# Kernel tuning notes

Measured on AMD Instinct MI355X. Metric: run time of the kernel, lower is better.

## Reference

```python
import jax, jax.numpy as jnp
import numpy as np

N = 4096       # number of graph nodes
F_IN = 512     # in_features == out_features (residual connection requires it)
H = 8          # n_heads


def setup_inputs() -> dict:
    key = jax.random.key(0)
    k1, k2, k3, k4, k5 = jax.random.split(key, 5)
    s = 1.0 / np.sqrt(F_IN)  # keep projections well-scaled
    x = jax.random.normal(k1, (N, F_IN), dtype=jnp.float32)
    Wq = jax.random.normal(k2, (F_IN, F_IN), dtype=jnp.float32) * s
    Wk = jax.random.normal(k3, (F_IN, F_IN), dtype=jnp.float32) * s
    Wv = jax.random.normal(k4, (F_IN, F_IN), dtype=jnp.float32) * s
    adj = jax.random.randint(k5, (H, N, N), 0, 2, dtype=jnp.int32)
    return {"x": x, "Wq": Wq, "Wk": Wk, "Wv": Wv, "adj": adj}


def reference(x, Wq, Wk, Wv, adj):
    # Faithful to torch GraphAttentionLayer.forward (eval mode, dropout off).
    # NOTE: the torch code builds keys = input.repeat(N,1,1).detach() -> the
    # K/V inputs are stop-gradient copies of x; projections are per-node, so
    # we compute them once instead of materializing the redundant [N,N,F].
    n, f = x.shape
    d = f // H  # head dim (chunk_size)
    xk = jax.lax.stop_gradient(x)
    # nn.Linear: y = x @ W.T ; split feature dim into heads -> [H, N, d]
    Q = (x @ Wq.T).reshape(n, H, d).transpose(1, 0, 2)
    K = (xk @ Wk.T).reshape(n, H, d).transpose(1, 0, 2)
    V = (xk @ Wv.T).reshape(n, H, d).transpose(1, 0, 2)
    # scaled by sqrt(in_features) (NOT head dim), as in the original
    scores = jnp.einsum('hnd,hmd->hnm', Q, K) / jnp.sqrt(jnp.float32(f))
    scores = jnp.where(adj > 0, scores, jnp.float32(-9e15))
    attn = jax.nn.softmax(scores, axis=-1)          # [H, N, N]
    out = jnp.einsum('hnm,hmd->hnd', attn, V)       # [H, N, d]
    out = out.transpose(1, 0, 2).reshape(n, f)      # concat heads -> [N, F]
    return jax.nn.elu(out + x)[:, None, :]          # [N, 1, F] like torch
```

## Files before the change

### kernel.cpp

```cpp
#include <hip/hip_runtime.h>
#include <hip/hip_bf16.h>

#define NN 4096
#define FF 512
#define NH 8
#define DH 64

typedef __attribute__((ext_vector_type(8))) short bf16x8;
typedef __attribute__((ext_vector_type(4))) float f32x4;

#define X_OFF  0
#define W_OFF  2097152
#define QF_OFF 2883584
#define KF_OFF 4980736
#define VF_OFF 7077888
#define PACC_OFF 9175040
#define PDEN_USHORT_OFF 17563648
#define PK_USHORT_OFF 17825792

__device__ __forceinline__ ushort f2bf(float f) {
    __hip_bfloat16 h = __float2bfloat16(f);
    return __builtin_bit_cast(ushort, h);
}
__device__ __forceinline__ float bf2f(ushort u) {
    unsigned int v = ((unsigned int)u) << 16;
    return __builtin_bit_cast(float, v);
}

__global__ __launch_bounds__(256) void cvt_kernel(const float* __restrict__ x,
                                                  const float* __restrict__ wq,
                                                  const float* __restrict__ wk,
                                                  const float* __restrict__ wv,
                                                  ushort* __restrict__ ws) {
    int i = blockIdx.x * 256 + threadIdx.x;
    int base = i * 4;
    const float* src;
    int off;
    float sc = 1.f;
    if (base < 2097152) { src = x; off = base; }
    else {
        int t = base - 2097152;
        int m = t >> 18;
        src = (m == 0) ? wq : ((m == 1) ? wk : wv);
        if (m == 0) sc = 0.044194173824159216f;
        off = t & 262143;
    }
    float4 v = *reinterpret_cast<const float4*>(src + off);
    ushort4 o;
    o.x = f2bf(v.x * sc); o.y = f2bf(v.y * sc); o.z = f2bf(v.z * sc); o.w = f2bf(v.w * sc);
    *reinterpret_cast<ushort4*>(ws + base) = o;
}

__global__ __launch_bounds__(256) void packqkv_kernel(const int* __restrict__ adj,
                                                      unsigned int* __restrict__ pk,
                                                      ushort* __restrict__ ws) {
    int bid = blockIdx.x;
    int wave = threadIdx.x >> 6, lane = threadIdx.x & 63;

    if (bid < 8192) {
        int row = bid * 4 + wave;
        const int* ar = adj + (size_t)row * 4096;
        unsigned long long* outp = reinterpret_cast<unsigned long long*>(pk + (size_t)row * 128);
        for (int it = 0; it < 64; it += 4) {
            int v0 = __builtin_nontemporal_load(ar + (it + 0) * 64 + lane);
            int v1 = __builtin_nontemporal_load(ar + (it + 1) * 64 + lane);
            int v2 = __builtin_nontemporal_load(ar + (it + 2) * 64 + lane);
            int v3 = __builtin_nontemporal_load(ar + (it + 3) * 64 + lane);
            unsigned long long b0 = __ballot(v0 != 0);
            unsigned long long b1 = __ballot(v1 != 0);
            unsigned long long b2 = __ballot(v2 != 0);
            unsigned long long b3 = __ballot(v3 != 0);
            if (lane == 0) {
                outp[it + 0] = b0;
                outp[it + 1] = b1;
                outp[it + 2] = b2;
                outp[it + 3] = b3;
            }
        }
        return;
    }

    int q = bid - 8192;
    int mat = q >> 9;
    int rem = q & 511;
    int fb = rem & 7;
    int mb = rem >> 3;
    int la = lane & 15, lk = lane >> 4;

    int m_base = mb * 64 + wave * 16;
    int f_base = fb * 64;

    const ushort* xb = ws + X_OFF;
    const ushort* wb = ws + W_OFF + mat * 262144;

    f32x4 acc[4];
#pragma unroll
    for (int t = 0; t < 4; ++t) acc[t] = (f32x4){0.f, 0.f, 0.f, 0.f};

#pragma unroll 4
    for (int k0 = 0; k0 < 512; k0 += 32) {
        bf16x8 a = *reinterpret_cast<const bf16x8*>(xb + (size_t)(m_base + la) * 512 + k0 + lk * 8);
#pragma unroll
        for (int ft = 0; ft < 4; ++ft) {
            bf16x8 b = *reinterpret_cast<const bf16x8*>(wb + (size_t)(f_base + ft * 16 + la) * 512 + k0 + lk * 8);
            acc[ft] = __builtin_amdgcn_mfma_f32_16x16x32_bf16(a, b, acc[ft], 0, 0, 0);
        }
    }

#pragma unroll
    for (int ft = 0; ft < 4; ++ft) {
#pragma unroll
        for (int r = 0; r < 4; ++r) {
            int n = m_base + lk * 4 + r;
            int d = ft * 16 + la;
            ushort v = f2bf(acc[ft][r]);
            if (mat < 2) {
                ushort* base = ws + (mat == 0 ? QF_OFF : KF_OFF) + (size_t)fb * 262144;
                int blk = n >> 4, rr = n & 15;
                int half = d >> 5, lkk = (d >> 3) & 3, e = d & 7;
                base[(((size_t)blk * 2 + half) * 64 + lkk * 16 + rr) * 8 + e] = v;
            } else {
                ushort* base = ws + VF_OFF + (size_t)fb * 262144;
                int kb64 = n >> 6, kc = n & 63;
                int hf = kc >> 5, lkv = (kc >> 3) & 3, ev = kc & 7;
                int dt = d >> 4, lav = d & 15;
                base[((((size_t)kb64 * 4 + dt) * 2 + hf) * 64 + lkv * 16 + lav) * 8 + ev] = v;
            }
        }
    }
}

__global__ __launch_bounds__(256, 4) void attn_kernel(const unsigned int* __restrict__ pk,
                                                      const ushort* __restrict__ ws,
                                                      ushort* __restrict__ pacc,
                                                      float* __restrict__ pden) {
    __shared__ ushort P[4][16][72];

    int bid = blockIdx.x;
    int h = bid & 7, qb = (bid >> 3) & 63, ks = bid >> 9;
    int wave = threadIdx.x >> 6, lane = threadIdx.x & 63;
    int la = lane & 15, lk = lane >> 4;
    int q0w = qb * 64 + wave * 16;

    const ushort* Qh = ws + QF_OFF + (size_t)h * 262144;
    const ushort* Kh = ws + KF_OFF + (size_t)h * 262144;
    const ushort* Vh = ws + VF_OFF + (size_t)h * 262144;
    const unsigned int* pkh = pk + (size_t)h * 4096 * 128;

    bf16x8 qa0 = *reinterpret_cast<const bf16x8*>(Qh + ((((size_t)(q0w >> 4)) * 2 + 0) * 64 + lane) * 8);
    bf16x8 qa1 = *reinterpret_cast<const bf16x8*>(Qh + ((((size_t)(q0w >> 4)) * 2 + 1) * 64 + lane) * 8);

    f32x4 acc[4];
    float den[4];
    int rowm[4];
#pragma unroll
    for (int r = 0; r < 4; ++r) {
        acc[r] = (f32x4){0.f, 0.f, 0.f, 0.f};
        den[r] = 0.f;
        rowm[r] = (q0w + lk * 4 + r) * 128;
    }

    const f32x4 zero = {0.f, 0.f, 0.f, 0.f};
    int kb0 = ks * 16;

    for (int it = 0; it < 16; ++it) {
        int kb = kb0 + it;

        uint2 mk[4];
#pragma unroll
        for (int r = 0; r < 4; ++r)
            mk[r] = *reinterpret_cast<const uint2*>(pkh + rowm[r] + kb * 2);

        f32x4 s[4];
#pragma unroll
        for (int kt = 0; kt < 4; ++kt) {
            const ushort* kp = Kh + (((size_t)(kb * 4 + kt) * 2) * 64 + lane) * 8;
            bf16x8 kf0 = *reinterpret_cast<const bf16x8*>(kp);
            bf16x8 kf1 = *reinterpret_cast<const bf16x8*>(kp + 512);
            s[kt] = __builtin_amdgcn_mfma_f32_16x16x32_bf16(qa0, kf0, zero, 0, 0, 0);
            s[kt] = __builtin_amdgcn_mfma_f32_16x16x32_bf16(qa1, kf1, s[kt], 0, 0, 0);
        }

#pragma unroll
        for (int kt = 0; kt < 4; ++kt) {
            int sh = la + ((kt & 1) << 4);
#pragma unroll
            for (int r = 0; r < 4; ++r) {
                unsigned int dw = (kt < 2) ? mk[r].x : mk[r].y;
                float sv = ((dw >> sh) & 1u) ? s[kt][r] : -1e30f;
                float e = __expf(sv);
                den[r] += e;
                P[wave][lk * 4 + r][kt * 16 + la] = f2bf(e);
            }
        }

        bf16x8 pa0 = *reinterpret_cast<const bf16x8*>(&P[wave][la][lk * 8]);
        bf16x8 pa1 = *reinterpret_cast<const bf16x8*>(&P[wave][la][32 + lk * 8]);
#pragma unroll
        for (int dt = 0; dt < 4; ++dt) {
            const ushort* vp = Vh + ((((size_t)kb * 4 + dt) * 2) * 64 + lane) * 8;
            bf16x8 vb0 = *reinterpret_cast<const bf16x8*>(vp);
            bf16x8 vb1 = *reinterpret_cast<const bf16x8*>(vp + 512);
            acc[dt] = __builtin_amdgcn_mfma_f32_16x16x32_bf16(pa0, vb0, acc[dt], 0, 0, 0);
            acc[dt] = __builtin_amdgcn_mfma_f32_16x16x32_bf16(pa1, vb1, acc[dt], 0, 0, 0);
        }
    }

#pragma unroll
    for (int r = 0; r < 4; ++r)
#pragma unroll
        for (int mm = 1; mm < 16; mm <<= 1)
            den[r] += __shfl_xor(den[r], mm, 64);

    ushort* pa_out = pacc + ((size_t)ks * 8 + h) * 4096 * 64;
#pragma unroll
    for (int dt = 0; dt < 4; ++dt)
#pragma unroll
        for (int r = 0; r < 4; ++r) {
            int qi = q0w + lk * 4 + r;
            __builtin_nontemporal_store(f2bf(acc[dt][r]), pa_out + (size_t)qi * 64 + dt * 16 + la);
        }
    if (la == 0) {
        float* pd = pden + ((size_t)ks * 8 + h) * 4096;
#pragma unroll
        for (int r = 0; r < 4; ++r)
            pd[q0w + lk * 4 + r] = den[r];
    }
}

__global__ __launch_bounds__(256) void combine_kernel(const float* __restrict__ x,
                                                      const ushort* __restrict__ pacc,
                                                      const float* __restrict__ pden,
                                                      float* __restrict__ out) {
    int idx = blockIdx.x * 256 + threadIdx.x;
    int n = idx >> 7, fq = idx & 127;
    int h = fq >> 4;
    int d4 = (fq & 15) * 4;

    float4 o = make_float4(0.f, 0.f, 0.f, 0.f);
    float den = 0.f;
#pragma unroll
    for (int ksp = 0; ksp < 4; ++ksp) {
        const ushort* pa = pacc + (((size_t)ksp * 8 + h) * 4096 + n) * 64 + d4;
        ushort4 p = *reinterpret_cast<const ushort4*>(pa);
        o.x += bf2f(p.x); o.y += bf2f(p.y); o.z += bf2f(p.z); o.w += bf2f(p.w);
        den += pden[((size_t)ksp * 8 + h) * 4096 + n];
    }
    float4 xv = *reinterpret_cast<const float4*>(x + (size_t)n * 512 + fq * 4);
    float inv = 1.f / den;
    float4 r;
    r.x = o.x * inv + xv.x;
    r.y = o.y * inv + xv.y;
    r.z = o.z * inv + xv.z;
    r.w = o.w * inv + xv.w;
    r.x = (r.x > 0.f) ? r.x : (__expf(r.x) - 1.f);
    r.y = (r.y > 0.f) ? r.y : (__expf(r.y) - 1.f);
    r.z = (r.z > 0.f) ? r.z : (__expf(r.z) - 1.f);
    r.w = (r.w > 0.f) ? r.w : (__expf(r.w) - 1.f);
    *reinterpret_cast<float4*>(out + (size_t)n * 512 + fq * 4) = r;
}

extern "C" void kernel_launch(void* const* d_in, const int* in_sizes, int n_in,
                              void* d_out, int out_size, void* d_ws, size_t ws_size,
                              hipStream_t stream) {
    const float* x  = (const float*)d_in[0];
    const float* wq = (const float*)d_in[1];
    const float* wk = (const float*)d_in[2];
    const float* wv = (const float*)d_in[3];
    const int*   adj = (const int*)d_in[4];
    float* out = (float*)d_out;
    ushort* ws = (ushort*)d_ws;
    ushort* pacc = ws + PACC_OFF;
    float* pden = (float*)(ws + PDEN_USHORT_OFF);
    unsigned int* pk = (unsigned int*)(ws + PK_USHORT_OFF);

    cvt_kernel<<<2816, 256, 0, stream>>>(x, wq, wk, wv, ws);
    packqkv_kernel<<<9728, 256, 0, stream>>>(adj, pk, ws);
    attn_kernel<<<2048, 256, 0, stream>>>(pk, ws, pacc, pden);
    combine_kernel<<<2048, 256, 0, stream>>>(x, pacc, pden, out);
}
```

Measured before the change: 250.0 us.

## Double-buffer K/V tiles in LDS via async global_load_lds and transpose score MFMA

K and V tiles for each key block, which all four waves share, are now loaded once per block into double-buffered shared memory with asynchronous global-to-LDS loads. The next block is prefetched while the current one is computed, replacing the per-wave global loads. The score MFMA operands are swapped so each lane holds four consecutive keys for one query row. That allows a single mask word load, a vectorized P store and a shorter denominator reduction. The cost is more LDS use, a lower occupancy bound (3 blocks per CU) and a block barrier every iteration.

```diff
diff --git a/kernel.cpp b/kernel.cpp
--- a/kernel.cpp
+++ b/kernel.cpp
@@ -130,10 +130,12 @@
     }
 }
 
-__global__ __launch_bounds__(256, 4) void attn_kernel(const unsigned int* __restrict__ pk,
+__global__ __launch_bounds__(256, 3) void attn_kernel(const unsigned int* __restrict__ pk,
                                                       const ushort* __restrict__ ws,
                                                       ushort* __restrict__ pacc,
                                                       float* __restrict__ pden) {
+    __shared__ ushort kbuf[2][8][512];
+    __shared__ ushort vbuf[2][8][512];
     __shared__ ushort P[4][16][72];
 
     int bid = blockIdx.x;
@@ -141,91 +143,99 @@
     int wave = threadIdx.x >> 6, lane = threadIdx.x & 63;
     int la = lane & 15, lk = lane >> 4;
     int q0w = qb * 64 + wave * 16;
+    int lk4 = lk * 4;
 
     const ushort* Qh = ws + QF_OFF + (size_t)h * 262144;
     const ushort* Kh = ws + KF_OFF + (size_t)h * 262144;
     const ushort* Vh = ws + VF_OFF + (size_t)h * 262144;
-    const unsigned int* pkh = pk + (size_t)h * 4096 * 128;
+    const unsigned int* mrow = pk + ((size_t)h * 4096 + q0w + la) * 128;
 
     bf16x8 qa0 = *reinterpret_cast<const bf16x8*>(Qh + ((((size_t)(q0w >> 4)) * 2 + 0) * 64 + lane) * 8);
     bf16x8 qa1 = *reinterpret_cast<const bf16x8*>(Qh + ((((size_t)(q0w >> 4)) * 2 + 1) * 64 + lane) * 8);
 
     f32x4 acc[4];
-    float den[4];
-    int rowm[4];
-#pragma unroll
-    for (int r = 0; r < 4; ++r) {
-        acc[r] = (f32x4){0.f, 0.f, 0.f, 0.f};
-        den[r] = 0.f;
-        rowm[r] = (q0w + lk * 4 + r) * 128;
-    }
+#pragma unroll
+    for (int r = 0; r < 4; ++r) acc[r] = (f32x4){0.f, 0.f, 0.f, 0.f};
+    float den = 0.f;
 
     const f32x4 zero = {0.f, 0.f, 0.f, 0.f};
     int kb0 = ks * 16;
 
+#define STAGE(BUF, KB)                                                                     \
+    {                                                                                      \
+        const ushort* sbase_ = (wave < 2) ? Kh : Vh;                                       \
+        ushort(*dbuf_)[512] = (wave < 2) ? kbuf[BUF] : vbuf[BUF];                          \
+        int t0_ = (wave & 1) * 4;                                                          \
+        _Pragma("unroll")                                                                  \
+        for (int t_ = 0; t_ < 4; ++t_) {                                                   \
+            int tile_ = t0_ + t_;                                                          \
+            const ushort* src_ = sbase_ +                                                  \
+                (((size_t)(KB) * 4 + (tile_ >> 1)) * 2 + (tile_ & 1)) * 512 + lane * 8;    \
+            __builtin_amdgcn_global_load_lds(                                              \
+                (const __attribute__((address_space(1))) unsigned int*)src_,               \
+                (__attribute__((address_space(3))) unsigned int*)&dbuf_[tile_][0],         \
+                16, 0, 0);                                                                 \
+        }                                                                                  \
+    }
+
+    STAGE(0, kb0)
+
     for (int it = 0; it < 16; ++it) {
         int kb = kb0 + it;
-
-        uint2 mk[4];
-#pragma unroll
-        for (int r = 0; r < 4; ++r)
-            mk[r] = *reinterpret_cast<const uint2*>(pkh + rowm[r] + kb * 2);
-
-        f32x4 s[4];
+        int cur = it & 1;
+
+        asm volatile("s_waitcnt vmcnt(0)" ::: "memory");
+        __builtin_amdgcn_s_barrier();
+
+        if (it < 15) STAGE(cur ^ 1, kb + 1)
+
+        uint2 mk = *reinterpret_cast<const uint2*>(mrow + kb * 2);
+
 #pragma unroll
         for (int kt = 0; kt < 4; ++kt) {
-            const ushort* kp = Kh + (((size_t)(kb * 4 + kt) * 2) * 64 + lane) * 8;
-            bf16x8 kf0 = *reinterpret_cast<const bf16x8*>(kp);
-            bf16x8 kf1 = *reinterpret_cast<const bf16x8*>(kp + 512);
-            s[kt] = __builtin_amdgcn_mfma_f32_16x16x32_bf16(qa0, kf0, zero, 0, 0, 0);
-            s[kt] = __builtin_amdgcn_mfma_f32_16x16x32_bf16(qa1, kf1, s[kt], 0, 0, 0);
-        }
-
-#pragma unroll
-        for (int kt = 0; kt < 4; ++kt) {
-            int sh = la + ((kt & 1) << 4);
-#pragma unroll
-            for (int r = 0; r < 4; ++r) {
-                unsigned int dw = (kt < 2) ? mk[r].x : mk[r].y;
-                float sv = ((dw >> sh) & 1u) ? s[kt][r] : -1e30f;
-                float e = __expf(sv);
-                den[r] += e;
-                P[wave][lk * 4 + r][kt * 16 + la] = f2bf(e);
-            }
+            bf16x8 kf0 = *reinterpret_cast<const bf16x8*>(&kbuf[cur][kt * 2 + 0][lane * 8]);
+            bf16x8 kf1 = *reinterpret_cast<const bf16x8*>(&kbuf[cur][kt * 2 + 1][lane * 8]);
+            f32x4 s = __builtin_amdgcn_mfma_f32_16x16x32_bf16(kf0, qa0, zero, 0, 0, 0);
+            s = __builtin_amdgcn_mfma_f32_16x16x32_bf16(kf1, qa1, s, 0, 0, 0);
+            unsigned int dw = (kt < 2) ? mk.x : mk.y;
+            int sh = ((kt & 1) << 4) + lk4;
+            ushort4 pw;
+            float e0 = __expf(((dw >> (sh + 0)) & 1u) ? s[0] : -1e30f);
+            float e1 = __expf(((dw >> (sh + 1)) & 1u) ? s[1] : -1e30f);
+            float e2 = __expf(((dw >> (sh + 2)) & 1u) ? s[2] : -1e30f);
+            float e3 = __expf(((dw >> (sh + 3)) & 1u) ? s[3] : -1e30f);
+            den += (e0 + e1) + (e2 + e3);
+            pw.x = f2bf(e0); pw.y = f2bf(e1); pw.z = f2bf(e2); pw.w = f2bf(e3);
+            *reinterpret_cast<ushort4*>(&P[wave][la][kt * 16 + lk4]) = pw;
         }
 
         bf16x8 pa0 = *reinterpret_cast<const bf16x8*>(&P[wave][la][lk * 8]);
         bf16x8 pa1 = *reinterpret_cast<const bf16x8*>(&P[wave][la][32 + lk * 8]);
 #pragma unroll
         for (int dt = 0; dt < 4; ++dt) {
-            const ushort* vp = Vh + ((((size_t)kb * 4 + dt) * 2) * 64 + lane) * 8;
-            bf16x8 vb0 = *reinterpret_cast<const bf16x8*>(vp);
-            bf16x8 vb1 = *reinterpret_cast<const bf16x8*>(vp + 512);
+            bf16x8 vb0 = *reinterpret_cast<const bf16x8*>(&vbuf[cur][dt * 2 + 0][lane * 8]);
+            bf16x8 vb1 = *reinterpret_cast<const bf16x8*>(&vbuf[cur][dt * 2 + 1][lane * 8]);
             acc[dt] = __builtin_amdgcn_mfma_f32_16x16x32_bf16(pa0, vb0, acc[dt], 0, 0, 0);
             acc[dt] = __builtin_amdgcn_mfma_f32_16x16x32_bf16(pa1, vb1, acc[dt], 0, 0, 0);
         }
     }
 
-#pragma unroll
-    for (int r = 0; r < 4; ++r)
-#pragma unroll
-        for (int mm = 1; mm < 16; mm <<= 1)
-            den[r] += __shfl_xor(den[r], mm, 64);
+    den += __shfl_xor(den, 16, 64);
+    den += __shfl_xor(den, 32, 64);
 
     ushort* pa_out = pacc + ((size_t)ks * 8 + h) * 4096 * 64;
 #pragma unroll
     for (int dt = 0; dt < 4; ++dt)
 #pragma unroll
         for (int r = 0; r < 4; ++r) {
-            int qi = q0w + lk * 4 + r;
+            int qi = q0w + lk4 + r;
             __builtin_nontemporal_store(f2bf(acc[dt][r]), pa_out + (size_t)qi * 64 + dt * 16 + la);
         }
-    if (la == 0) {
+    if (lane < 16) {
         float* pd = pden + ((size_t)ks * 8 + h) * 4096;
-#pragma unroll
-        for (int r = 0; r < 4; ++r)
-            pd[q0w + lk * 4 + r] = den[r];
-    }
+        pd[q0w + lane] = den;
+    }
+#undef STAGE
 }
 
 __global__ __launch_bounds__(256) void combine_kernel(const float* __restrict__ x,
```

Result: faster. 226.8 us (-9.2%).
